# Kernel tuning notes

Measured on AMD Instinct MI355X. Metric: run time of the kernel, lower is better.

Reference implementation:

```python
import jax, jax.numpy as jnp
import numpy as np

WS = 8            # window_size
SHIFT = WS // 2   # shift_size


def _relative_position_index(ws):
    coords = np.stack(np.meshgrid(np.arange(ws), np.arange(ws), indexing='ij'))  # (2, ws, ws)
    coords = coords.reshape(2, -1)                        # (2, ws^2)
    rel = coords[:, :, None] - coords[:, None, :]          # (2, ws^2, ws^2)
    rel = rel.transpose(1, 2, 0)
    rel[:, :, 0] += ws - 1
    rel[:, :, 1] += ws - 1
    rel[:, :, 0] *= 2 * ws - 1
    return rel.sum(-1).astype(np.int32)                   # (ws^2, ws^2)


def _shift_mask(H, W, ws, shift):
    # Swin-style region-id mask for shifted windows -> bool (nh, nw, ws^2, ws^2)
    img = np.zeros((H, W), dtype=np.int32)
    cnt = 0
    sl = (slice(0, -ws), slice(-ws, -shift), slice(-shift, None))
    for hs in sl:
        for wsl in sl:
            img[hs, wsl] = cnt
            cnt += 1
    nh, nw = H // ws, W // ws
    win = img.reshape(nh, ws, nw, ws).transpose(0, 2, 1, 3).reshape(nh, nw, ws * ws)
    return win[:, :, :, None] != win[:, :, None, :]


def setup_inputs() -> dict:
    key = jax.random.key(0)
    ks = jax.random.split(key, 6)
    B, H, W, D, NHEAD = 8, 256, 256, 96, 6
    x = jax.random.normal(ks[0], (B, H, W, D), dtype=jnp.float32)
    w_qkv = jax.random.normal(ks[1], (D, 3 * D), dtype=jnp.float32) * 0.05
    b_qkv = jnp.zeros((3 * D,), dtype=jnp.float32)
    w_out = jax.random.normal(ks[2], (D, D), dtype=jnp.float32) * 0.05
    b_out = jnp.zeros((D,), dtype=jnp.float32)
    rpe_table = jax.random.normal(ks[3], ((2 * WS - 1) ** 2, NHEAD), dtype=jnp.float32) * 0.02
    rp_index = jnp.asarray(_relative_position_index(WS))
    mask = jnp.asarray(_shift_mask(H, W, WS, SHIFT))
    return {"x": x, "w_qkv": w_qkv, "b_qkv": b_qkv, "w_out": w_out,
            "b_out": b_out, "rpe_table": rpe_table, "rp_index": rp_index, "mask": mask}


def _partition(t, ws):
    # (B, h, H, W, dk) -> (B, h, nh, nw, ws*ws, dk)
    B, h, H, W, dk = t.shape
    nh, nw = H // ws, W // ws
    t = t.reshape(B, h, nh, ws, nw, ws, dk).transpose(0, 1, 2, 4, 3, 5, 6)
    return t.reshape(B, h, nh, nw, ws * ws, dk)


def _merge(t, ws):
    # inverse of _partition -> (B, h, H, W, dk)
    B, h, nh, nw, _, dk = t.shape
    t = t.reshape(B, h, nh, nw, ws, ws, dk).transpose(0, 1, 2, 4, 3, 5, 6)
    return t.reshape(B, h, nh * ws, nw * ws, dk)


def reference(x, w_qkv, b_qkv, w_out, b_out, rpe_table, rp_index, mask):
    B, H, W, D = x.shape
    n_head = rpe_table.shape[1]
    d_k = D // n_head
    scale = 1.0 / np.sqrt(d_k)
    ws2 = mask.shape[-1]
    ws = int(round(ws2 ** 0.5))
    shift = ws // 2

    qkv = (x @ w_qkv + b_qkv).reshape(B, H, W, 3, n_head, d_k)
    qkv = qkv.transpose(3, 0, 4, 1, 2, 5)          # (3, B, h, H, W, dk)
    q, k, v = qkv[0], qkv[1], qkv[2]

    # cyclic shift
    q = jnp.roll(q, (-shift, -shift), axis=(2, 3))
    k = jnp.roll(k, (-shift, -shift), axis=(2, 3))
    v = jnp.roll(v, (-shift, -shift), axis=(2, 3))

    q = _partition(q, ws)                          # (B, h, nh, nw, ws^2, dk)
    k = _partition(k, ws)
    v = _partition(v, ws)

    scores = jnp.einsum('bhijqd,bhijkd->bhijqk', q, k) * scale
    bias = rpe_table[rp_index]                     # (ws^2, ws^2, h)
    scores = scores + bias.transpose(2, 0, 1)[None, :, None, None]
    scores = jnp.where(mask[None, None], -1e9, scores)
    attn = jax.nn.softmax(scores, axis=-1)

    out = jnp.einsum('bhijqk,bhijkd->bhijqd', attn, v)
    out = _merge(out, ws)                          # (B, h, H, W, dk)
    out = jnp.roll(out, (shift, shift), axis=(2, 3))
    out = out.transpose(0, 2, 3, 1, 4).reshape(B, H, W, D)
    return out @ w_out + b_out
```

## Files before the change

kernel.cpp:

```cpp
#include <hip/hip_runtime.h>
#include <stdint.h>

#define HH    256
#define DD    96
#define NH    6
#define WSZ   8

typedef __bf16 bf16_t;
typedef bf16_t bf16x8 __attribute__((ext_vector_type(8)));
typedef short  s16x4  __attribute__((ext_vector_type(4)));
typedef float  f32x4  __attribute__((ext_vector_type(4)));

union U2  { bf16_t h[2]; uint32_t u; };
union Upk { uint32_t u[2]; s16x4 s; };

#define LOG2E 1.44269504088896f

static __device__ __forceinline__ uint32_t pack2(float a, float b) {
    U2 x; x.h[0] = (bf16_t)a; x.h[1] = (bf16_t)b; return x.u;
}

static __device__ __forceinline__ f32x4 mfma16(s16x4 a, s16x4 b, f32x4 c) {
#if __has_builtin(__builtin_amdgcn_mfma_f32_16x16x16bf16_1k)
    return __builtin_amdgcn_mfma_f32_16x16x16bf16_1k(a, b, c, 0, 0, 0);
#else
    f32x4 d;
    asm volatile("v_mfma_f32_16x16x16_bf16 %0, %1, %2, %3"
                 : "=v"(d) : "v"(a), "v"(b), "v"(c));
    return d;
#endif
}

static __device__ __forceinline__ float fast_exp2(float x) {
#if __has_builtin(__builtin_amdgcn_exp2f)
    return __builtin_amdgcn_exp2f(x);
#else
    return exp2f(x);
#endif
}

static __device__ __forceinline__ float fast_rcp(float x) {
#if __has_builtin(__builtin_amdgcn_rcpf)
    return __builtin_amdgcn_rcpf(x);
#else
    return 1.0f / x;
#endif
}

#define OFF_WQT_HI 0
#define OFF_WQT_LO 36864
#define OFF_WV_HI  73728
#define OFF_WV_LO  92160
#define OFF_WO_HI  110592
#define OFF_WO_LO  129024
#define OFF_RPE    147456

static __device__ __forceinline__ int swz(int row, int col) {
    return row * 128 + ((((col >> 3) ^ (row & 15)) & 15) << 3) + (col & 7);
}

__global__ __launch_bounds__(256)
void prep_kernel(const float* __restrict__ wqkv, const float* __restrict__ wout,
                 const float* __restrict__ rpe, char* __restrict__ ws)
{
    bf16_t* wqt_hi = (bf16_t*)(ws + OFF_WQT_HI);
    bf16_t* wqt_lo = (bf16_t*)(ws + OFF_WQT_LO);
    bf16_t* wv_hi  = (bf16_t*)(ws + OFF_WV_HI);
    bf16_t* wv_lo  = (bf16_t*)(ws + OFF_WV_LO);
    bf16_t* wo_hi  = (bf16_t*)(ws + OFF_WO_HI);
    bf16_t* wo_lo  = (bf16_t*)(ws + OFF_WO_LO);
    float*  rpe_b  = (float*)(ws + OFF_RPE);

    int idx = blockIdx.x * 256 + threadIdx.x;
    {
        int j = idx & 7, lane = (idx >> 3) & 63, frag = idx >> 9;
        int c = lane & 15, g = lane >> 4;
        if (idx < 18432) {
            int ks = frag % 3, r2 = frag / 3, wh = r2 % 6, t = r2 / 6;
            int k = ks * 32 + g * 8 + j;
            float v = wqkv[k * 288 + t * 96 + wh * 16 + c];
            bf16_t h = (bf16_t)v;
            wqt_hi[idx] = h;
            wqt_lo[idx] = (bf16_t)(v - (float)h);
        }
        if (idx < 9216) {
            int ks = frag % 3, wh = frag / 3;
            int k = ks * 32 + g * 8 + j;
            float v = wqkv[k * 288 + 192 + wh * 16 + c];
            bf16_t h = (bf16_t)v;
            wv_hi[idx] = h;
            wv_lo[idx] = (bf16_t)(v - (float)h);
            float v2 = wout[k * 96 + wh * 16 + c];
            bf16_t h2 = (bf16_t)v2;
            wo_hi[idx] = h2;
            wo_lo[idx] = (bf16_t)(v2 - (float)h2);
        }
    }
    if (idx < 24576) {
        int i = idx & 3, lane = (idx >> 2) & 63, kt = (idx >> 8) & 3,
            nt = (idx >> 10) & 3, h = idx >> 12;
        int c = lane & 15, g = lane >> 4;
        int k = kt * 16 + g * 4 + i, q = nt * 16 + c;
        int qr = q >> 3, qc = q & 7, kr = k >> 3, kc = k & 7;
        rpe_b[idx] = rpe[((qr - kr + 7) * 15 + (qc - kc + 7)) * NH + h] * LOG2E;
    }
}

__global__ __launch_bounds__(768, 4)
void swin_mfma(const float* __restrict__ x,
               const float* __restrict__ b_qkv,
               const float* __restrict__ b_out,
               const char*  __restrict__ ws,
               float* __restrict__ out)
{
    __shared__ char smem[65536];

    const int tid  = threadIdx.x;
    const int w2   = tid >> 6;
    const int wv   = (w2 >= 6) ? 1 : 0;
    const int w    = w2 - 6 * wv;
    const int lane = tid & 63;
    const int g    = lane >> 4;
    const int c    = lane & 15;
    const int tl   = tid - (wv << 8) - (wv << 7);

    bf16_t* xs_hi = (bf16_t*)(smem + (wv << 14));
    bf16_t* o_hi  = (bf16_t*)(smem + 32768 + (wv << 14));

    const bf16_t* wqt_hi = (const bf16_t*)(ws + OFF_WQT_HI);
    const bf16_t* wqt_lo = (const bf16_t*)(ws + OFF_WQT_LO);
    const bf16_t* wv_hi  = (const bf16_t*)(ws + OFF_WV_HI);
    const bf16_t* wv_lo  = (const bf16_t*)(ws + OFF_WV_LO);
    const bf16_t* wo_hi  = (const bf16_t*)(ws + OFF_WO_HI);
    const bf16_t* wo_lo  = (const bf16_t*)(ws + OFF_WO_LO);
    const float*  rpe_b  = (const float*)(ws + OFF_RPE);

    const int blk = blockIdx.x;
    const int b   = blk >> 9;
    const int wi  = (blk >> 4) & 31;
    const int wj  = ((blk & 15) << 1) + wv;

    uint32_t pix[4];
    #pragma unroll
    for (int t = 0; t < 4; ++t) {
        int p = t * 16 + c;
        int gh = (wi * WSZ + (p >> 3) + 4) & 255;
        int gw = (wj * WSZ + (p & 7) + 4) & 255;
        pix[t] = (((uint32_t)b * HH + gh) << 8) + gw;
    }

    const f32x4 zf = {0.f, 0.f, 0.f, 0.f};

    #pragma unroll
    for (int it = 0; it < 4; ++it) {
        int f4  = tl + it * 384;
        int row = f4 / 24, c4 = f4 - row * 24;
        int r = row >> 3, cl = row & 7;
        int gh = (wi * WSZ + r + 4) & 255;
        int gw = (wj * WSZ + cl + 4) & 255;
        const float4 v = *(const float4*)(x + (((size_t)b * HH + gh) * HH + gw) * DD + c4 * 4);
        uint2 hv;
        hv.x = pack2(v.x, v.y); hv.y = pack2(v.z, v.w);
        *(uint2*)&xs_hi[swz(row, c4 * 4)] = hv;
    }
    __syncthreads();

    f32x4 aq[4], akk[4], av[4];
    {
        const float4 bq4 = *(const float4*)&b_qkv[w * 16 + 4 * g];
        const float4 bk4 = *(const float4*)&b_qkv[96 + w * 16 + 4 * g];
        const float  bv  = b_qkv[192 + w * 16 + c];
        #pragma unroll
        for (int t4 = 0; t4 < 4; ++t4) {
            aq[t4]  = (f32x4){bq4.x, bq4.y, bq4.z, bq4.w};
            akk[t4] = (f32x4){bk4.x, bk4.y, bk4.z, bk4.w};
            av[t4]  = (f32x4){bv, bv, bv, bv};
        }
    }
    #pragma unroll
    for (int ks = 0; ks < 3; ++ks) {
        bf16x8 ah[4];
        #pragma unroll
        for (int mt = 0; mt < 4; ++mt) {
            int e = (mt * 16 + c) * 128 + (((ks * 4 + g) ^ c) << 3);
            ah[mt] = *(const bf16x8*)&xs_hi[e];
        }
        const bf16x8 qh = *(const bf16x8*)&wqt_hi[(w * 3 + ks) * 512 + lane * 8];
        const bf16x8 ql = *(const bf16x8*)&wqt_lo[(w * 3 + ks) * 512 + lane * 8];
        const bf16x8 kh = *(const bf16x8*)&wqt_hi[((6 + w) * 3 + ks) * 512 + lane * 8];
        const bf16x8 kl = *(const bf16x8*)&wqt_lo[((6 + w) * 3 + ks) * 512 + lane * 8];
        const bf16x8 vh = *(const bf16x8*)&wv_hi[(w * 3 + ks) * 512 + lane * 8];
        const bf16x8 vl = *(const bf16x8*)&wv_lo[(w * 3 + ks) * 512 + lane * 8];
        #pragma unroll
        for (int mt = 0; mt < 4; ++mt) {
            aq[mt]  = __builtin_amdgcn_mfma_f32_16x16x32_bf16(qh, ah[mt], aq[mt], 0, 0, 0);
            aq[mt]  = __builtin_amdgcn_mfma_f32_16x16x32_bf16(ql, ah[mt], aq[mt], 0, 0, 0);
            akk[mt] = __builtin_amdgcn_mfma_f32_16x16x32_bf16(kh, ah[mt], akk[mt], 0, 0, 0);
            akk[mt] = __builtin_amdgcn_mfma_f32_16x16x32_bf16(kl, ah[mt], akk[mt], 0, 0, 0);
            av[mt]  = __builtin_amdgcn_mfma_f32_16x16x32_bf16(ah[mt], vh, av[mt], 0, 0, 0);
            av[mt]  = __builtin_amdgcn_mfma_f32_16x16x32_bf16(ah[mt], vl, av[mt], 0, 0, 0);
        }
    }

    s16x4 aqb[4], akb[4], avb[4];
    #pragma unroll
    for (int t = 0; t < 4; ++t) {
        Upk uq, uk, uv;
        const float qs = 0.25f * LOG2E;
        uq.u[0] = pack2(aq[t][0] * qs, aq[t][1] * qs);
        uq.u[1] = pack2(aq[t][2] * qs, aq[t][3] * qs);
        uk.u[0] = pack2(akk[t][0], akk[t][1]);
        uk.u[1] = pack2(akk[t][2], akk[t][3]);
        uv.u[0] = pack2(av[t][0], av[t][1]);
        uv.u[1] = pack2(av[t][2], av[t][3]);
        aqb[t] = uq.s; akb[t] = uk.s; avb[t] = uv.s;
    }

    const int e_wi = (wi == 31), e_wj = (wj == 31);
    const bool edge = e_wi || e_wj;
    int rk[4][4];
    #pragma unroll
    for (int kt = 0; kt < 4; ++kt)
        #pragma unroll
        for (int i = 0; i < 4; ++i) {
            int k = kt * 16 + g * 4 + i;
            int kr = k >> 3, kc = k & 7;
            rk[kt][i] = (e_wi ? (kr >= 4 ? 2 : 1) : 0) * 3 + (e_wj ? (kc >= 4 ? 2 : 1) : 0);
        }

    #pragma unroll
    for (int nt = 0; nt < 4; ++nt) {
        f32x4 stc[4];
        #pragma unroll
        for (int kt = 0; kt < 4; ++kt) {
            const f32x4 rc = *(const f32x4*)&rpe_b[(((w * 4 + nt) * 4 + kt) << 8) + lane * 4];
            stc[kt] = mfma16(akb[kt], aqb[nt], rc);
        }

        int q = nt * 16 + c, qr = q >> 3, qc = q & 7;
        int rq = (e_wi ? (qr >= 4 ? 2 : 1) : 0) * 3 + (e_wj ? (qc >= 4 ? 2 : 1) : 0);
        float sv[16];
        float sum = 0.f;
        #pragma unroll
        for (int kt = 0; kt < 4; ++kt)
            #pragma unroll
            for (int i = 0; i < 4; ++i) {
                float s = stc[kt][i];
                if (edge && (rk[kt][i] != rq)) s = -1e9f;
                s = fast_exp2(s);
                sv[kt * 4 + i] = s;
                sum += s;
            }
        sum += __shfl_xor(sum, 16);
        sum += __shfl_xor(sum, 32);
        const float rinv = fast_rcp(sum);

        f32x4 oa = zf;
        #pragma unroll
        for (int ks2 = 0; ks2 < 4; ++ks2) {
            Upk pb;
            pb.u[0] = pack2(sv[ks2 * 4 + 0], sv[ks2 * 4 + 1]);
            pb.u[1] = pack2(sv[ks2 * 4 + 2], sv[ks2 * 4 + 3]);
            oa = mfma16(avb[ks2], pb.s, oa);
        }
        {
            uint2 hv;
            hv.x = pack2(oa[0] * rinv, oa[1] * rinv);
            hv.y = pack2(oa[2] * rinv, oa[3] * rinv);
            *(uint2*)&o_hi[swz(nt * 16 + c, w * 16 + 4 * g)] = hv;
        }
    }
    __syncthreads();

    f32x4 acc3[4];
    {
        const float4 bo4 = *(const float4*)&b_out[w * 16 + 4 * g];
        #pragma unroll
        for (int nt = 0; nt < 4; ++nt)
            acc3[nt] = (f32x4){bo4.x, bo4.y, bo4.z, bo4.w};
    }
    #pragma unroll
    for (int ks = 0; ks < 3; ++ks) {
        bf16x8 oh[4];
        #pragma unroll
        for (int nt = 0; nt < 4; ++nt) {
            int e = (nt * 16 + c) * 128 + (((ks * 4 + g) ^ c) << 3);
            oh[nt] = *(const bf16x8*)&o_hi[e];
        }
        const bf16x8 bh = *(const bf16x8*)&wo_hi[(w * 3 + ks) * 512 + lane * 8];
        const bf16x8 bl = *(const bf16x8*)&wo_lo[(w * 3 + ks) * 512 + lane * 8];
        #pragma unroll
        for (int nt = 0; nt < 4; ++nt) {
            acc3[nt] = __builtin_amdgcn_mfma_f32_16x16x32_bf16(bh, oh[nt], acc3[nt], 0, 0, 0);
            acc3[nt] = __builtin_amdgcn_mfma_f32_16x16x32_bf16(bl, oh[nt], acc3[nt], 0, 0, 0);
        }
    }
    #pragma unroll
    for (int nt = 0; nt < 4; ++nt)
        *(f32x4*)(out + (size_t)pix[nt] * DD + w * 16 + 4 * g) = acc3[nt];
}

extern "C" void kernel_launch(void* const* d_in, const int* in_sizes, int n_in,
                              void* d_out, int out_size, void* d_ws, size_t ws_size,
                              hipStream_t stream) {
    const float* x    = (const float*)d_in[0];
    const float* wqkv = (const float*)d_in[1];
    const float* bqkv = (const float*)d_in[2];
    const float* wout = (const float*)d_in[3];
    const float* bout = (const float*)d_in[4];
    const float* rpe  = (const float*)d_in[5];
    float* out = (float*)d_out;
    char* ws = (char*)d_ws;

    const int B = in_sizes[0] / (HH * HH * DD);

    hipLaunchKernelGGL(prep_kernel, dim3(96), dim3(256), 0, stream, wqkv, wout, rpe, ws);
    hipLaunchKernelGGL(swin_mfma, dim3(B * 512), dim3(768), 0, stream,
                       x, bqkv, bout, (const char*)ws, out);
}
```

Before: 194.8 us.

## Split fused Swin kernel into LDS-free attention and out-projection kernels

Replaces the single fused kernel with two kernels when the workspace is large enough. The first computes QKV and windowed attention, reading x directly from global memory into MFMA fragments without LDS staging, and writes the per-window bf16 attention output to a workspace buffer. The second performs the output projection from that buffer. This removes shared memory use and block-wide barriers so more blocks can be resident, at the cost of an extra global round trip for the intermediate, an additional launch, and less coalesced loads of x.

```diff
diff --git a/kernel.cpp b/kernel.cpp
--- a/kernel.cpp
+++ b/kernel.cpp
@@ -12,6 +12,7 @@
 typedef float  f32x4  __attribute__((ext_vector_type(4)));
 
 union U2  { bf16_t h[2]; uint32_t u; };
+union U4  { bf16x8 v; uint32_t u[4]; };
 union Upk { uint32_t u[2]; s16x4 s; };
 
 #define LOG2E 1.44269504088896f
@@ -54,6 +55,7 @@
 #define OFF_WO_HI  110592
 #define OFF_WO_LO  129024
 #define OFF_RPE    147456
+#define OFF_O      262144
 
 static __device__ __forceinline__ int swz(int row, int col) {
     return row * 128 + ((((col >> 3) ^ (row & 15)) & 15) << 3) + (col & 7);
@@ -106,39 +108,28 @@
     }
 }
 
-__global__ __launch_bounds__(768, 4)
-void swin_mfma(const float* __restrict__ x,
-               const float* __restrict__ b_qkv,
-               const float* __restrict__ b_out,
-               const char*  __restrict__ ws,
-               float* __restrict__ out)
+__global__ __launch_bounds__(384, 4)
+void swin_qkv_attn(const float* __restrict__ x,
+                   const float* __restrict__ b_qkv,
+                   char* __restrict__ ws)
 {
-    __shared__ char smem[65536];
-
     const int tid  = threadIdx.x;
-    const int w2   = tid >> 6;
-    const int wv   = (w2 >= 6) ? 1 : 0;
-    const int w    = w2 - 6 * wv;
+    const int w    = tid >> 6;
     const int lane = tid & 63;
     const int g    = lane >> 4;
     const int c    = lane & 15;
-    const int tl   = tid - (wv << 8) - (wv << 7);
-
-    bf16_t* xs_hi = (bf16_t*)(smem + (wv << 14));
-    bf16_t* o_hi  = (bf16_t*)(smem + 32768 + (wv << 14));
 
     const bf16_t* wqt_hi = (const bf16_t*)(ws + OFF_WQT_HI);
     const bf16_t* wqt_lo = (const bf16_t*)(ws + OFF_WQT_LO);
     const bf16_t* wv_hi  = (const bf16_t*)(ws + OFF_WV_HI);
     const bf16_t* wv_lo  = (const bf16_t*)(ws + OFF_WV_LO);
-    const bf16_t* wo_hi  = (const bf16_t*)(ws + OFF_WO_HI);
-    const bf16_t* wo_lo  = (const bf16_t*)(ws + OFF_WO_LO);
     const float*  rpe_b  = (const float*)(ws + OFF_RPE);
+    bf16_t* o_ws = (bf16_t*)(ws + OFF_O);
 
     const int blk = blockIdx.x;
-    const int b   = blk >> 9;
-    const int wi  = (blk >> 4) & 31;
-    const int wj  = ((blk & 15) << 1) + wv;
+    const int b   = blk >> 10;
+    const int wi  = (blk >> 5) & 31;
+    const int wj  = blk & 31;
 
     uint32_t pix[4];
     #pragma unroll
@@ -151,20 +142,6 @@
 
     const f32x4 zf = {0.f, 0.f, 0.f, 0.f};
 
-    #pragma unroll
-    for (int it = 0; it < 4; ++it) {
-        int f4  = tl + it * 384;
-        int row = f4 / 24, c4 = f4 - row * 24;
-        int r = row >> 3, cl = row & 7;
-        int gh = (wi * WSZ + r + 4) & 255;
-        int gw = (wj * WSZ + cl + 4) & 255;
-        const float4 v = *(const float4*)(x + (((size_t)b * HH + gh) * HH + gw) * DD + c4 * 4);
-        uint2 hv;
-        hv.x = pack2(v.x, v.y); hv.y = pack2(v.z, v.w);
-        *(uint2*)&xs_hi[swz(row, c4 * 4)] = hv;
-    }
-    __syncthreads();
-
     f32x4 aq[4], akk[4], av[4];
     {
         const float4 bq4 = *(const float4*)&b_qkv[w * 16 + 4 * g];
@@ -182,8 +159,13 @@
         bf16x8 ah[4];
         #pragma unroll
         for (int mt = 0; mt < 4; ++mt) {
-            int e = (mt * 16 + c) * 128 + (((ks * 4 + g) ^ c) << 3);
-            ah[mt] = *(const bf16x8*)&xs_hi[e];
+            const float* xp = x + (size_t)pix[mt] * DD + ks * 32 + g * 8;
+            const float4 lo = *(const float4*)xp;
+            const float4 hi = *(const float4*)(xp + 4);
+            U4 u;
+            u.u[0] = pack2(lo.x, lo.y); u.u[1] = pack2(lo.z, lo.w);
+            u.u[2] = pack2(hi.x, hi.y); u.u[3] = pack2(hi.z, hi.w);
+            ah[mt] = u.v;
         }
         const bf16x8 qh = *(const bf16x8*)&wqt_hi[(w * 3 + ks) * 512 + lane * 8];
         const bf16x8 ql = *(const bf16x8*)&wqt_lo[(w * 3 + ks) * 512 + lane * 8];
@@ -227,6 +209,8 @@
             int kr = k >> 3, kc = k & 7;
             rk[kt][i] = (e_wi ? (kr >= 4 ? 2 : 1) : 0) * 3 + (e_wj ? (kc >= 4 ? 2 : 1) : 0);
         }
+
+    bf16_t* owin = o_ws + (size_t)blk * (64 * DD);
 
     #pragma unroll
     for (int nt = 0; nt < 4; ++nt) {
@@ -263,12 +247,230 @@
             pb.u[1] = pack2(sv[ks2 * 4 + 2], sv[ks2 * 4 + 3]);
             oa = mfma16(avb[ks2], pb.s, oa);
         }
-        {
-            uint2 hv;
-            hv.x = pack2(oa[0] * rinv, oa[1] * rinv);
-            hv.y = pack2(oa[2] * rinv, oa[3] * rinv);
-            *(uint2*)&o_hi[swz(nt * 16 + c, w * 16 + 4 * g)] = hv;
-        }
+        uint2 hv;
+        hv.x = pack2(oa[0] * rinv, oa[1] * rinv);
+        hv.y = pack2(oa[2] * rinv, oa[3] * rinv);
+        *(uint2*)&owin[(nt * 16 + c) * DD + w * 16 + 4 * g] = hv;
+    }
+}
+
+__global__ __launch_bounds__(384, 4)
+void swin_outproj(const float* __restrict__ b_out,
+                  const char* __restrict__ ws,
+                  float* __restrict__ out)
+{
+    const int tid  = threadIdx.x;
+    const int w    = tid >> 6;
+    const int lane = tid & 63;
+    const int g    = lane >> 4;
+    const int c    = lane & 15;
+
+    const bf16_t* wo_hi = (const bf16_t*)(ws + OFF_WO_HI);
+    const bf16_t* wo_lo = (const bf16_t*)(ws + OFF_WO_LO);
+    const bf16_t* o_ws  = (const bf16_t*)(ws + OFF_O);
+
+    const int blk = blockIdx.x;
+    const int b   = blk >> 10;
+    const int wi  = (blk >> 5) & 31;
+    const int wj  = blk & 31;
+
+    uint32_t pix[4];
+    #pragma unroll
+    for (int t = 0; t < 4; ++t) {
+        int p = t * 16 + c;
+        int gh = (wi * WSZ + (p >> 3) + 4) & 255;
+        int gw = (wj * WSZ + (p & 7) + 4) & 255;
+        pix[t] = (((uint32_t)b * HH + gh) << 8) + gw;
+    }
+
+    const bf16_t* owin = o_ws + (size_t)blk * (64 * DD);
+
+    f32x4 acc3[4];
+    {
+        const float4 bo4 = *(const float4*)&b_out[w * 16 + 4 * g];
+        #pragma unroll
+        for (int nt = 0; nt < 4; ++nt)
+            acc3[nt] = (f32x4){bo4.x, bo4.y, bo4.z, bo4.w};
+    }
+    #pragma unroll
+    for (int ks = 0; ks < 3; ++ks) {
+        bf16x8 oh[4];
+        #pragma unroll
+        for (int nt = 0; nt < 4; ++nt)
+            oh[nt] = *(const bf16x8*)&owin[(nt * 16 + c) * DD + ks * 32 + g * 8];
+        const bf16x8 bh = *(const bf16x8*)&wo_hi[(w * 3 + ks) * 512 + lane * 8];
+        const bf16x8 bl = *(const bf16x8*)&wo_lo[(w * 3 + ks) * 512 + lane * 8];
+        #pragma unroll
+        for (int nt = 0; nt < 4; ++nt) {
+            acc3[nt] = __builtin_amdgcn_mfma_f32_16x16x32_bf16(bh, oh[nt], acc3[nt], 0, 0, 0);
+            acc3[nt] = __builtin_amdgcn_mfma_f32_16x16x32_bf16(bl, oh[nt], acc3[nt], 0, 0, 0);
+        }
+    }
+    #pragma unroll
+    for (int nt = 0; nt < 4; ++nt)
+        *(f32x4*)(out + (size_t)pix[nt] * DD + w * 16 + 4 * g) = acc3[nt];
+}
+
+__global__ __launch_bounds__(768, 4)
+void swin_fused(const float* __restrict__ x,
+                const float* __restrict__ b_qkv,
+                const float* __restrict__ b_out,
+                const char*  __restrict__ ws,
+                float* __restrict__ out)
+{
+    __shared__ char smem[65536];
+
+    const int tid  = threadIdx.x;
+    const int w2   = tid >> 6;
+    const int wv   = (w2 >= 6) ? 1 : 0;
+    const int w    = w2 - 6 * wv;
+    const int lane = tid & 63;
+    const int g    = lane >> 4;
+    const int c    = lane & 15;
+    const int tl   = tid - (wv << 8) - (wv << 7);
+
+    bf16_t* xs_hi = (bf16_t*)(smem + (wv << 14));
+    bf16_t* o_hi  = (bf16_t*)(smem + 32768 + (wv << 14));
+
+    const bf16_t* wqt_hi = (const bf16_t*)(ws + OFF_WQT_HI);
+    const bf16_t* wqt_lo = (const bf16_t*)(ws + OFF_WQT_LO);
+    const bf16_t* wv_hi  = (const bf16_t*)(ws + OFF_WV_HI);
+    const bf16_t* wv_lo  = (const bf16_t*)(ws + OFF_WV_LO);
+    const bf16_t* wo_hi  = (const bf16_t*)(ws + OFF_WO_HI);
+    const bf16_t* wo_lo  = (const bf16_t*)(ws + OFF_WO_LO);
+    const float*  rpe_b  = (const float*)(ws + OFF_RPE);
+
+    const int blk = blockIdx.x;
+    const int b   = blk >> 9;
+    const int wi  = (blk >> 4) & 31;
+    const int wj  = ((blk & 15) << 1) + wv;
+
+    uint32_t pix[4];
+    #pragma unroll
+    for (int t = 0; t < 4; ++t) {
+        int p = t * 16 + c;
+        int gh = (wi * WSZ + (p >> 3) + 4) & 255;
+        int gw = (wj * WSZ + (p & 7) + 4) & 255;
+        pix[t] = (((uint32_t)b * HH + gh) << 8) + gw;
+    }
+
+    const f32x4 zf = {0.f, 0.f, 0.f, 0.f};
+
+    #pragma unroll
+    for (int it = 0; it < 4; ++it) {
+        int f4  = tl + it * 384;
+        int row = f4 / 24, c4 = f4 - row * 24;
+        int r = row >> 3, cl = row & 7;
+        int gh = (wi * WSZ + r + 4) & 255;
+        int gw = (wj * WSZ + cl + 4) & 255;
+        const float4 v = *(const float4*)(x + (((size_t)b * HH + gh) * HH + gw) * DD + c4 * 4);
+        uint2 hv;
+        hv.x = pack2(v.x, v.y); hv.y = pack2(v.z, v.w);
+        *(uint2*)&xs_hi[swz(row, c4 * 4)] = hv;
+    }
+    __syncthreads();
+
+    f32x4 aq[4], akk[4], av[4];
+    {
+        const float4 bq4 = *(const float4*)&b_qkv[w * 16 + 4 * g];
+        const float4 bk4 = *(const float4*)&b_qkv[96 + w * 16 + 4 * g];
+        const float  bv  = b_qkv[192 + w * 16 + c];
+        #pragma unroll
+        for (int t4 = 0; t4 < 4; ++t4) {
+            aq[t4]  = (f32x4){bq4.x, bq4.y, bq4.z, bq4.w};
+            akk[t4] = (f32x4){bk4.x, bk4.y, bk4.z, bk4.w};
+            av[t4]  = (f32x4){bv, bv, bv, bv};
+        }
+    }
+    #pragma unroll
+    for (int ks = 0; ks < 3; ++ks) {
+        bf16x8 ah[4];
+        #pragma unroll
+        for (int mt = 0; mt < 4; ++mt) {
+            int e = (mt * 16 + c) * 128 + (((ks * 4 + g) ^ c) << 3);
+            ah[mt] = *(const bf16x8*)&xs_hi[e];
+        }
+        const bf16x8 qh = *(const bf16x8*)&wqt_hi[(w * 3 + ks) * 512 + lane * 8];
+        const bf16x8 ql = *(const bf16x8*)&wqt_lo[(w * 3 + ks) * 512 + lane * 8];
+        const bf16x8 kh = *(const bf16x8*)&wqt_hi[((6 + w) * 3 + ks) * 512 + lane * 8];
+        const bf16x8 kl = *(const bf16x8*)&wqt_lo[((6 + w) * 3 + ks) * 512 + lane * 8];
+        const bf16x8 vh = *(const bf16x8*)&wv_hi[(w * 3 + ks) * 512 + lane * 8];
+        const bf16x8 vl = *(const bf16x8*)&wv_lo[(w * 3 + ks) * 512 + lane * 8];
+        #pragma unroll
+        for (int mt = 0; mt < 4; ++mt) {
+            aq[mt]  = __builtin_amdgcn_mfma_f32_16x16x32_bf16(qh, ah[mt], aq[mt], 0, 0, 0);
+            aq[mt]  = __builtin_amdgcn_mfma_f32_16x16x32_bf16(ql, ah[mt], aq[mt], 0, 0, 0);
+            akk[mt] = __builtin_amdgcn_mfma_f32_16x16x32_bf16(kh, ah[mt], akk[mt], 0, 0, 0);
+            akk[mt] = __builtin_amdgcn_mfma_f32_16x16x32_bf16(kl, ah[mt], akk[mt], 0, 0, 0);
+            av[mt]  = __builtin_amdgcn_mfma_f32_16x16x32_bf16(ah[mt], vh, av[mt], 0, 0, 0);
+            av[mt]  = __builtin_amdgcn_mfma_f32_16x16x32_bf16(ah[mt], vl, av[mt], 0, 0, 0);
+        }
+    }
+
+    s16x4 aqb[4], akb[4], avb[4];
+    #pragma unroll
+    for (int t = 0; t < 4; ++t) {
+        Upk uq, uk, uv;
+        const float qs = 0.25f * LOG2E;
+        uq.u[0] = pack2(aq[t][0] * qs, aq[t][1] * qs);
+        uq.u[1] = pack2(aq[t][2] * qs, aq[t][3] * qs);
+        uk.u[0] = pack2(akk[t][0], akk[t][1]);
+        uk.u[1] = pack2(akk[t][2], akk[t][3]);
+        uv.u[0] = pack2(av[t][0], av[t][1]);
+        uv.u[1] = pack2(av[t][2], av[t][3]);
+        aqb[t] = uq.s; akb[t] = uk.s; avb[t] = uv.s;
+    }
+
+    const int e_wi = (wi == 31), e_wj = (wj == 31);
+    const bool edge = e_wi || e_wj;
+    int rk[4][4];
+    #pragma unroll
+    for (int kt = 0; kt < 4; ++kt)
+        #pragma unroll
+        for (int i = 0; i < 4; ++i) {
+            int k = kt * 16 + g * 4 + i;
+            int kr = k >> 3, kc = k & 7;
+            rk[kt][i] = (e_wi ? (kr >= 4 ? 2 : 1) : 0) * 3 + (e_wj ? (kc >= 4 ? 2 : 1) : 0);
+        }
+
+    #pragma unroll
+    for (int nt = 0; nt < 4; ++nt) {
+        f32x4 stc[4];
+        #pragma unroll
+        for (int kt = 0; kt < 4; ++kt) {
+            const f32x4 rc = *(const f32x4*)&rpe_b[(((w * 4 + nt) * 4 + kt) << 8) + lane * 4];
+            stc[kt] = mfma16(akb[kt], aqb[nt], rc);
+        }
+        int q = nt * 16 + c, qr = q >> 3, qc = q & 7;
+        int rq = (e_wi ? (qr >= 4 ? 2 : 1) : 0) * 3 + (e_wj ? (qc >= 4 ? 2 : 1) : 0);
+        float sv[16];
+        float sum = 0.f;
+        #pragma unroll
+        for (int kt = 0; kt < 4; ++kt)
+            #pragma unroll
+            for (int i = 0; i < 4; ++i) {
+                float s = stc[kt][i];
+                if (edge && (rk[kt][i] != rq)) s = -1e9f;
+                s = fast_exp2(s);
+                sv[kt * 4 + i] = s;
+                sum += s;
+            }
+        sum += __shfl_xor(sum, 16);
+        sum += __shfl_xor(sum, 32);
+        const float rinv = fast_rcp(sum);
+
+        f32x4 oa = zf;
+        #pragma unroll
+        for (int ks2 = 0; ks2 < 4; ++ks2) {
+            Upk pb;
+            pb.u[0] = pack2(sv[ks2 * 4 + 0], sv[ks2 * 4 + 1]);
+            pb.u[1] = pack2(sv[ks2 * 4 + 2], sv[ks2 * 4 + 3]);
+            oa = mfma16(avb[ks2], pb.s, oa);
+        }
+        uint2 hv;
+        hv.x = pack2(oa[0] * rinv, oa[1] * rinv);
+        hv.y = pack2(oa[2] * rinv, oa[3] * rinv);
+        *(uint2*)&o_hi[swz(nt * 16 + c, w * 16 + 4 * g)] = hv;
     }
     __syncthreads();
 
@@ -313,8 +515,14 @@
     char* ws = (char*)d_ws;
 
     const int B = in_sizes[0] / (HH * HH * DD);
+    const size_t o_need = (size_t)OFF_O + (size_t)B * 1024 * 64 * DD * sizeof(bf16_t);
 
     hipLaunchKernelGGL(prep_kernel, dim3(96), dim3(256), 0, stream, wqkv, wout, rpe, ws);
-    hipLaunchKernelGGL(swin_mfma, dim3(B * 512), dim3(768), 0, stream,
-                       x, bqkv, bout, (const char*)ws, out);
-}
+    if (ws_size >= o_need) {
+        hipLaunchKernelGGL(swin_qkv_attn, dim3(B * 1024), dim3(384), 0, stream, x, bqkv, ws);
+        hipLaunchKernelGGL(swin_outproj,  dim3(B * 1024), dim3(384), 0, stream, bout, (const char*)ws, out);
+    } else {
+        hipLaunchKernelGGL(swin_fused, dim3(B * 512), dim3(768), 0, stream,
+                           x, bqkv, bout, (const char*)ws, out);
+    }
+}
```

New measurement: 383.1 us. 96.7% more time.
